# Kernel tuning notes

Measured on AMD Instinct MI355X. Metric: run time of the kernel, lower is better.

The kernel has to match this reference:

```python
import jax, jax.numpy as jnp
import numpy as np

N_NODES = 2048


def setup_inputs() -> dict:
    key = jax.random.key(0)
    ks = jax.random.split(key, 9)
    N, IN, HID, OUT, R, B1 = N_NODES, 64, 32, 16, 4, 1
    s = 0.1
    return {
        "x": jax.random.normal(ks[0], (N, IN), jnp.float32),
        # adj_initial = ones - eye, as in __init__ (learnable parameter)
        "adj_matrix": jnp.ones((N, N), jnp.float32) - jnp.eye(N, dtype=jnp.float32),
        "bases1": jax.random.normal(ks[1], (B1, IN, HID), jnp.float32) * s,
        "coeff1": jax.random.normal(ks[2], (R, B1), jnp.float32) * s,
        "loop_w1": jax.random.normal(ks[3], (IN, HID), jnp.float32) * s,
        "bias1": jnp.zeros((HID,), jnp.float32),
        "bases2": jax.random.normal(ks[4], (R, HID, OUT), jnp.float32) * s,
        "coeff2": jax.random.normal(ks[5], (R, R), jnp.float32) * s,
        "loop_w2": jax.random.normal(ks[6], (HID, OUT), jnp.float32) * s,
        "bias2": jnp.zeros((OUT,), jnp.float32),
        "edge_type": 0,  # ignored by the module (etype is rebuilt as zeros)
    }


def _rel_graph_conv(h, bases, coeff, loop_w, bias, src, dst, n_nodes, act):
    # basis regularizer: W_r = sum_b coeff[r, b] * bases[b]; all edges have etype 0
    W0 = jnp.einsum('b,bio->io', coeff[0], bases)          # [in, out]
    msg = (h @ W0)[src]                                    # [E, out] gather-by-edge
    agg = jax.ops.segment_sum(msg, dst, num_segments=n_nodes)  # scatter-sum
    out = agg + h @ loop_w + bias                          # self-loop + bias
    return act(out)


def reference(x, adj_matrix, bases1, coeff1, loop_w1, bias1,
              bases2, coeff2, loop_w2, bias2, edge_type):
    N = x.shape[0]
    # sigmoid(adj_matrix) > 0 everywhere (sigmoid(0)=0.5 on the diagonal), so
    # torch.nonzero yields ALL N^2 pairs in row-major order: complete graph
    # with self-loops. Structure is static -> build edges with arange.
    idx = jnp.arange(N)
    src = jnp.repeat(idx, N)   # [N*N]
    dst = jnp.tile(idx, N)     # [N*N]
    h = _rel_graph_conv(x, bases1, coeff1, loop_w1, bias1, src, dst, N, jax.nn.relu)
    h = _rel_graph_conv(h, bases2, coeff2, loop_w2, bias2, src, dst, N, lambda z: z)
    return h
```

## Files before the change

kernel.cpp:

```cpp
#include <hip/hip_runtime.h>

#define NN 2048
#define IN 64
#define HID 32
#define OUTD 16


__global__ __launch_bounds__(256) void k_colsum_x(const float* __restrict__ x,
                                                  float* __restrict__ ws) {
    __shared__ float part[256];
    int tid = threadIdx.x;
    int col = tid & 63;
    int sub = tid >> 6;
    int r0 = blockIdx.x * 8 + sub;
    float p = x[r0 * IN + col] + x[(r0 + 4) * IN + col];
    part[tid] = p;
    __syncthreads();
    if (tid < 64) {
        float s = part[tid] + part[tid + 64] + part[tid + 128] + part[tid + 192];
        atomicAdd(&ws[tid], s);
    }
}

__device__ inline void compute_agg1(const float* s0sh, const float* __restrict__ bases1,
                                    const float* __restrict__ bias1, float c1,
                                    float* agg1sh, float* scratch, int tid) {
    int h = tid & 31, seg = tid >> 5;
    float p = 0.f;
#pragma unroll
    for (int k = 0; k < 8; ++k)
        p += s0sh[seg * 8 + k] * bases1[(seg * 8 + k) * HID + h];
    scratch[tid] = p;
    __syncthreads();
    if (tid < HID) {
        float s = 0.f;
#pragma unroll
        for (int s2 = 0; s2 < 8; ++s2) s += scratch[s2 * 32 + tid];
        agg1sh[tid] = bias1[tid] + c1 * s;
    }
}

__global__ __launch_bounds__(256) void k_layer1(const float* __restrict__ x,
                                                const float* __restrict__ bases1,
                                                const float* __restrict__ coeff1,
                                                const float* __restrict__ loop_w1,
                                                const float* __restrict__ bias1,
                                                float* __restrict__ ws) {
    __shared__ float w1sh[IN * HID];
    __shared__ float xsh[8 * IN];
    __shared__ float s0sh[IN];
    __shared__ float agg1sh[HID];
    __shared__ float scratch[256];
    int tid = threadIdx.x;
    int b = blockIdx.x;
    for (int idx = tid; idx < IN * HID; idx += 256) w1sh[idx] = loop_w1[idx];
    for (int idx = tid; idx < 8 * IN; idx += 256) xsh[idx] = x[b * 8 * IN + idx];
    if (tid < IN) s0sh[tid] = ws[tid];
    __syncthreads();
    float c1 = coeff1[0];
    compute_agg1(s0sh, bases1, bias1, c1, agg1sh, scratch, tid);
    __syncthreads();
    int rib = tid >> 5, col = tid & 31;
    float acc = agg1sh[col];
#pragma unroll
    for (int k = 0; k < IN; ++k) acc += xsh[rib * IN + k] * w1sh[k * HID + col];
    acc = fmaxf(acc, 0.f);
    __syncthreads();
    scratch[tid] = acc;
    __syncthreads();
    if (tid < HID) {
        float s = 0.f;
#pragma unroll
        for (int r = 0; r < 8; ++r) s += scratch[r * 32 + tid];
        atomicAdd(&ws[64 + tid], s);
    }
}

__global__ __launch_bounds__(256) void k_layer2(const float* __restrict__ x,
                                                const float* __restrict__ bases1,
                                                const float* __restrict__ coeff1,
                                                const float* __restrict__ loop_w1,
                                                const float* __restrict__ bias1,
                                                const float* __restrict__ bases2,
                                                const float* __restrict__ coeff2,
                                                const float* __restrict__ loop_w2,
                                                const float* __restrict__ bias2,
                                                const float* __restrict__ ws,
                                                float* __restrict__ out) {
    __shared__ float w1sh[IN * HID];
    __shared__ float xsh[16 * IN];
    __shared__ float s0sh[IN];
    __shared__ float s1sh[HID];
    __shared__ float agg1sh[HID];
    __shared__ float w2csh[HID * OUTD];
    __shared__ float w2sh[HID * OUTD];
    __shared__ float agg2sh[OUTD];
    __shared__ float h1sh[16 * 33];
    __shared__ float scratch[256];
    int tid = threadIdx.x;
    int b = blockIdx.x;
    for (int idx = tid; idx < IN * HID; idx += 256) w1sh[idx] = loop_w1[idx];
    for (int idx = tid; idx < 16 * IN; idx += 256) xsh[idx] = x[b * 16 * IN + idx];
    for (int idx = tid; idx < HID * OUTD; idx += 256) w2sh[idx] = loop_w2[idx];
    if (tid < IN) s0sh[tid] = ws[tid];
    if (tid >= 64 && tid < 96) s1sh[tid - 64] = ws[tid];
    float c20 = coeff2[0], c21 = coeff2[1], c22 = coeff2[2], c23 = coeff2[3];
    for (int idx = tid; idx < HID * OUTD; idx += 256)
        w2csh[idx] = c20 * bases2[idx] + c21 * bases2[512 + idx] +
                     c22 * bases2[1024 + idx] + c23 * bases2[1536 + idx];
    __syncthreads();
    float c1 = coeff1[0];
    compute_agg1(s0sh, bases1, bias1, c1, agg1sh, scratch, tid);
    if (tid >= 32 && tid < 48) {
        int o = tid - 32;
        float s = 0.f;
#pragma unroll
        for (int h = 0; h < HID; ++h) s += s1sh[h] * w2csh[h * OUTD + o];
        agg2sh[o] = bias2[o] + s;
    }
    __syncthreads();
    for (int idx = tid; idx < 16 * HID; idx += 256) {
        int row = idx >> 5, h = idx & 31;
        float acc = agg1sh[h];
#pragma unroll
        for (int k = 0; k < IN; ++k) acc += xsh[row * IN + k] * w1sh[k * HID + h];
        h1sh[row * 33 + h] = fmaxf(acc, 0.f);
    }
    __syncthreads();
    int rib = tid >> 4, o = tid & 15;
    float acc = agg2sh[o];
#pragma unroll
    for (int h = 0; h < HID; ++h) acc += h1sh[rib * 33 + h] * w2sh[h * OUTD + o];
    out[b * 256 + tid] = acc;
}

extern "C" void kernel_launch(void* const* d_in, const int* in_sizes, int n_in,
                              void* d_out, int out_size, void* d_ws, size_t ws_size,
                              hipStream_t stream) {
    const float* x       = (const float*)d_in[0];
    const float* bases1  = (const float*)d_in[2];
    const float* coeff1  = (const float*)d_in[3];
    const float* loop_w1 = (const float*)d_in[4];
    const float* bias1   = (const float*)d_in[5];
    const float* bases2  = (const float*)d_in[6];
    const float* coeff2  = (const float*)d_in[7];
    const float* loop_w2 = (const float*)d_in[8];
    const float* bias2   = (const float*)d_in[9];
    float* out = (float*)d_out;
    float* ws  = (float*)d_ws;

    hipMemsetAsync(d_ws, 0, 96 * sizeof(float), stream);
    k_colsum_x<<<256, 256, 0, stream>>>(x, ws);
    k_layer1<<<256, 256, 0, stream>>>(x, bases1, coeff1, loop_w1, bias1, ws);
    k_layer2<<<128, 256, 0, stream>>>(x, bases1, coeff1, loop_w1, bias1,
                                      bases2, coeff2, loop_w2, bias2, ws, out);
}
```

Measured before the change: 103.0 us.

## Fuse RGCN pipeline into single cooperative kernel with grid syncs

Replaces the memset and three separate kernels with one cooperative kernel of 64 blocks. Two grid-wide syncs separate the column-sum of x, the layer-1 row computation with its h1 column sums, and the layer-2 output. Atomics are replaced by per-block partial sums written to the workspace and then reduced redundantly by every block. Layer-1 activations stay in shared memory instead of being recomputed in the second pass. The aim is to remove launch overhead and redundant work, at the cost of grid-sync latency and fewer, larger blocks.

```diff
diff --git a/kernel.cpp b/kernel.cpp
--- a/kernel.cpp
+++ b/kernel.cpp
@@ -1,137 +1,154 @@
 #include <hip/hip_runtime.h>
+#include <hip/hip_cooperative_groups.h>
 
-#define NN 2048
-#define IN 64
-#define HID 32
+namespace cg = cooperative_groups;
+
+#define NN   2048
+#define IN   64
+#define HID  32
 #define OUTD 16
+#define NB   64
+#define RPB  32
 
+#define XPART_OFF  0
+#define H1PART_OFF (NB * IN)
 
-__global__ __launch_bounds__(256) void k_colsum_x(const float* __restrict__ x,
-                                                  float* __restrict__ ws) {
-    __shared__ float part[256];
-    int tid = threadIdx.x;
-    int col = tid & 63;
-    int sub = tid >> 6;
-    int r0 = blockIdx.x * 8 + sub;
-    float p = x[r0 * IN + col] + x[(r0 + 4) * IN + col];
-    part[tid] = p;
-    __syncthreads();
-    if (tid < 64) {
-        float s = part[tid] + part[tid + 64] + part[tid + 128] + part[tid + 192];
-        atomicAdd(&ws[tid], s);
-    }
-}
+__global__ __launch_bounds__(256) void rgcn_fused(
+    const float* __restrict__ x,
+    const float* __restrict__ bases1,
+    const float* __restrict__ coeff1,
+    const float* __restrict__ loop_w1,
+    const float* __restrict__ bias1,
+    const float* __restrict__ bases2,
+    const float* __restrict__ coeff2,
+    const float* __restrict__ loop_w2,
+    const float* __restrict__ bias2,
+    float* __restrict__ ws,
+    float* __restrict__ out)
+{
+    cg::grid_group grid = cg::this_grid();
 
-__device__ inline void compute_agg1(const float* s0sh, const float* __restrict__ bases1,
-                                    const float* __restrict__ bias1, float c1,
-                                    float* agg1sh, float* scratch, int tid) {
-    int h = tid & 31, seg = tid >> 5;
-    float p = 0.f;
-#pragma unroll
-    for (int k = 0; k < 8; ++k)
-        p += s0sh[seg * 8 + k] * bases1[(seg * 8 + k) * HID + h];
-    scratch[tid] = p;
-    __syncthreads();
-    if (tid < HID) {
-        float s = 0.f;
-#pragma unroll
-        for (int s2 = 0; s2 < 8; ++s2) s += scratch[s2 * 32 + tid];
-        agg1sh[tid] = bias1[tid] + c1 * s;
-    }
-}
-
-__global__ __launch_bounds__(256) void k_layer1(const float* __restrict__ x,
-                                                const float* __restrict__ bases1,
-                                                const float* __restrict__ coeff1,
-                                                const float* __restrict__ loop_w1,
-                                                const float* __restrict__ bias1,
-                                                float* __restrict__ ws) {
+    __shared__ float xsh[RPB * IN];
     __shared__ float w1sh[IN * HID];
-    __shared__ float xsh[8 * IN];
-    __shared__ float s0sh[IN];
-    __shared__ float agg1sh[HID];
-    __shared__ float scratch[256];
-    int tid = threadIdx.x;
-    int b = blockIdx.x;
-    for (int idx = tid; idx < IN * HID; idx += 256) w1sh[idx] = loop_w1[idx];
-    for (int idx = tid; idx < 8 * IN; idx += 256) xsh[idx] = x[b * 8 * IN + idx];
-    if (tid < IN) s0sh[tid] = ws[tid];
-    __syncthreads();
-    float c1 = coeff1[0];
-    compute_agg1(s0sh, bases1, bias1, c1, agg1sh, scratch, tid);
-    __syncthreads();
-    int rib = tid >> 5, col = tid & 31;
-    float acc = agg1sh[col];
-#pragma unroll
-    for (int k = 0; k < IN; ++k) acc += xsh[rib * IN + k] * w1sh[k * HID + col];
-    acc = fmaxf(acc, 0.f);
-    __syncthreads();
-    scratch[tid] = acc;
-    __syncthreads();
-    if (tid < HID) {
-        float s = 0.f;
-#pragma unroll
-        for (int r = 0; r < 8; ++r) s += scratch[r * 32 + tid];
-        atomicAdd(&ws[64 + tid], s);
-    }
-}
-
-__global__ __launch_bounds__(256) void k_layer2(const float* __restrict__ x,
-                                                const float* __restrict__ bases1,
-                                                const float* __restrict__ coeff1,
-                                                const float* __restrict__ loop_w1,
-                                                const float* __restrict__ bias1,
-                                                const float* __restrict__ bases2,
-                                                const float* __restrict__ coeff2,
-                                                const float* __restrict__ loop_w2,
-                                                const float* __restrict__ bias2,
-                                                const float* __restrict__ ws,
-                                                float* __restrict__ out) {
-    __shared__ float w1sh[IN * HID];
-    __shared__ float xsh[16 * IN];
+    __shared__ float w2sh[HID * OUTD];
+    __shared__ float w2csh[HID * OUTD];
+    __shared__ float h1sh[RPB * (HID + 1)];
     __shared__ float s0sh[IN];
     __shared__ float s1sh[HID];
     __shared__ float agg1sh[HID];
-    __shared__ float w2csh[HID * OUTD];
-    __shared__ float w2sh[HID * OUTD];
     __shared__ float agg2sh[OUTD];
-    __shared__ float h1sh[16 * 33];
     __shared__ float scratch[256];
-    int tid = threadIdx.x;
-    int b = blockIdx.x;
-    for (int idx = tid; idx < IN * HID; idx += 256) w1sh[idx] = loop_w1[idx];
-    for (int idx = tid; idx < 16 * IN; idx += 256) xsh[idx] = x[b * 16 * IN + idx];
-    for (int idx = tid; idx < HID * OUTD; idx += 256) w2sh[idx] = loop_w2[idx];
-    if (tid < IN) s0sh[tid] = ws[tid];
-    if (tid >= 64 && tid < 96) s1sh[tid - 64] = ws[tid];
-    float c20 = coeff2[0], c21 = coeff2[1], c22 = coeff2[2], c23 = coeff2[3];
-    for (int idx = tid; idx < HID * OUTD; idx += 256)
-        w2csh[idx] = c20 * bases2[idx] + c21 * bases2[512 + idx] +
-                     c22 * bases2[1024 + idx] + c23 * bases2[1536 + idx];
+
+    const int tid = threadIdx.x;
+    const int b   = blockIdx.x;
+
+    for (int idx = tid; idx < RPB * IN; idx += 256)
+        xsh[idx] = x[b * RPB * IN + idx];
+    for (int idx = tid; idx < IN * HID; idx += 256)
+        w1sh[idx] = loop_w1[idx];
+    {
+        const float c20 = coeff2[0], c21 = coeff2[1], c22 = coeff2[2], c23 = coeff2[3];
+        for (int idx = tid; idx < HID * OUTD; idx += 256) {
+            w2sh[idx]  = loop_w2[idx];
+            w2csh[idx] = c20 * bases2[idx]        + c21 * bases2[512 + idx] +
+                         c22 * bases2[1024 + idx] + c23 * bases2[1536 + idx];
+        }
+    }
     __syncthreads();
-    float c1 = coeff1[0];
-    compute_agg1(s0sh, bases1, bias1, c1, agg1sh, scratch, tid);
-    if (tid >= 32 && tid < 48) {
-        int o = tid - 32;
+
+    {
+        const int col = tid & 63, grp = tid >> 6;
+        float p = 0.f;
+#pragma unroll
+        for (int r = 0; r < 8; ++r)
+            p += xsh[(grp * 8 + r) * IN + col];
+        scratch[tid] = p;
+        __syncthreads();
+        if (tid < IN)
+            ws[XPART_OFF + b * IN + tid] =
+                scratch[tid] + scratch[tid + 64] + scratch[tid + 128] + scratch[tid + 192];
+    }
+
+    grid.sync();
+
+    if (tid < IN) {
+        float s = 0.f;
+        for (int blk = 0; blk < NB; ++blk)
+            s += ws[XPART_OFF + blk * IN + tid];
+        s0sh[tid] = s;
+    }
+    __syncthreads();
+
+    {
+        const float c1 = coeff1[0];
+        const int h = tid & 31, seg = tid >> 5;
+        float p = 0.f;
+#pragma unroll
+        for (int k = 0; k < 8; ++k)
+            p += s0sh[seg * 8 + k] * bases1[(seg * 8 + k) * HID + h];
+        scratch[tid] = p;
+        __syncthreads();
+        if (tid < HID) {
+            float s = 0.f;
+#pragma unroll
+            for (int s2 = 0; s2 < 8; ++s2) s += scratch[s2 * 32 + tid];
+            agg1sh[tid] = bias1[tid] + c1 * s;
+        }
+    }
+    __syncthreads();
+
+    for (int idx = tid; idx < RPB * HID; idx += 256) {
+        const int row = idx >> 5, h = idx & 31;
+        float acc = agg1sh[h];
+#pragma unroll
+        for (int k = 0; k < IN; ++k)
+            acc += xsh[row * IN + k] * w1sh[k * HID + h];
+        h1sh[row * (HID + 1) + h] = fmaxf(acc, 0.f);
+    }
+    __syncthreads();
+
+    {
+        const int h = tid & 31, grp = tid >> 5;
+        float q = 0.f;
+#pragma unroll
+        for (int r = 0; r < 4; ++r)
+            q += h1sh[(grp * 4 + r) * (HID + 1) + h];
+        scratch[tid] = q;
+        __syncthreads();
+        if (tid < HID) {
+            float s = 0.f;
+#pragma unroll
+            for (int g = 0; g < 8; ++g) s += scratch[g * 32 + tid];
+            ws[H1PART_OFF + b * HID + tid] = s;
+        }
+    }
+
+    grid.sync();
+
+    if (tid < HID) {
+        float s = 0.f;
+        for (int blk = 0; blk < NB; ++blk)
+            s += ws[H1PART_OFF + blk * HID + tid];
+        s1sh[tid] = s;
+    }
+    __syncthreads();
+    if (tid < OUTD) {
         float s = 0.f;
 #pragma unroll
-        for (int h = 0; h < HID; ++h) s += s1sh[h] * w2csh[h * OUTD + o];
-        agg2sh[o] = bias2[o] + s;
+        for (int h = 0; h < HID; ++h)
+            s += s1sh[h] * w2csh[h * OUTD + tid];
+        agg2sh[tid] = bias2[tid] + s;
     }
     __syncthreads();
-    for (int idx = tid; idx < 16 * HID; idx += 256) {
-        int row = idx >> 5, h = idx & 31;
-        float acc = agg1sh[h];
+
+    for (int idx = tid; idx < RPB * OUTD; idx += 256) {
+        const int row = idx >> 4, o = idx & 15;
+        float acc = agg2sh[o];
 #pragma unroll
-        for (int k = 0; k < IN; ++k) acc += xsh[row * IN + k] * w1sh[k * HID + h];
-        h1sh[row * 33 + h] = fmaxf(acc, 0.f);
+        for (int h = 0; h < HID; ++h)
+            acc += h1sh[row * (HID + 1) + h] * w2sh[h * OUTD + o];
+        out[b * RPB * OUTD + idx] = acc;
     }
-    __syncthreads();
-    int rib = tid >> 4, o = tid & 15;
-    float acc = agg2sh[o];
-#pragma unroll
-    for (int h = 0; h < HID; ++h) acc += h1sh[rib * 33 + h] * w2sh[h * OUTD + o];
-    out[b * 256 + tid] = acc;
 }
 
 extern "C" void kernel_launch(void* const* d_in, const int* in_sizes, int n_in,
@@ -149,9 +166,11 @@
     float* out = (float*)d_out;
     float* ws  = (float*)d_ws;
 
-    hipMemsetAsync(d_ws, 0, 96 * sizeof(float), stream);
-    k_colsum_x<<<256, 256, 0, stream>>>(x, ws);
-    k_layer1<<<256, 256, 0, stream>>>(x, bases1, coeff1, loop_w1, bias1, ws);
-    k_layer2<<<128, 256, 0, stream>>>(x, bases1, coeff1, loop_w1, bias1,
-                                      bases2, coeff2, loop_w2, bias2, ws, out);
+    void* args[] = {
+        (void*)&x, (void*)&bases1, (void*)&coeff1, (void*)&loop_w1, (void*)&bias1,
+        (void*)&bases2, (void*)&coeff2, (void*)&loop_w2, (void*)&bias2,
+        (void*)&ws, (void*)&out
+    };
+    hipLaunchCooperativeKernel((const void*)rgcn_fused, dim3(NB), dim3(256),
+                               args, 0, stream);
 }
```

New measurement: 130.7 us. 1.27x slower.
